# Performance work log

Measured on AMD Instinct MI355X. Metric: run time of the kernel, lower is better.

The kernel has to match this reference:

```python
import jax, jax.numpy as jnp
import numpy as np

V, CTX, D, L, H = 50257, 2048, 768, 12, 12
HD = D // H
EPS = 1e-5


def _ln(x, w, b):
    mu = jnp.mean(x, axis=-1, keepdims=True)
    var = jnp.mean(jnp.square(x - mu), axis=-1, keepdims=True)
    return (x - mu) * jax.lax.rsqrt(var + EPS) * w + b


def setup_inputs() -> dict:
    key = jax.random.key(0)
    ks = jax.random.split(key, 8)
    s = 0.02  # init std, matches _init_weights
    return {
        "idx": jax.random.randint(ks[0], (2, 2048), 0, V),
        "wte": jax.random.normal(ks[1], (V, D), jnp.float32) * s,
        "wpe": jax.random.normal(ks[2], (CTX, D), jnp.float32) * s,
        "ln1_w": jnp.ones((L, D), jnp.float32),
        "ln1_b": jnp.zeros((L, D), jnp.float32),
        "qkv_w": jax.random.normal(ks[3], (L, 3 * D, D), jnp.float32) * s,
        "out_w": jax.random.normal(ks[4], (L, D, D), jnp.float32) * s,
        "ln2_w": jnp.ones((L, D), jnp.float32),
        "ln2_b": jnp.zeros((L, D), jnp.float32),
        "fc1_w": jax.random.normal(ks[5], (L, 4 * D, D), jnp.float32) * s,
        "fc2_w": jax.random.normal(ks[6], (L, D, 4 * D), jnp.float32) * s,
        "lnf_w": jnp.ones((D,), jnp.float32),
        "lnf_b": jnp.zeros((D,), jnp.float32),
    }


def reference(idx, wte, wpe, ln1_w, ln1_b, qkv_w, out_w, ln2_w, ln2_b,
              fc1_w, fc2_w, lnf_w, lnf_b):
    B, S = idx.shape
    x = wte[idx] + wpe[:S][None]  # [B,S,D]
    causal = jnp.tril(jnp.ones((S, S), bool))  # [S,S]
    scale = 1.0 / np.sqrt(HD)

    def block(x, p):
        l1w, l1b, qkvw, ow, l2w, l2b, f1w, f2w = p
        h = _ln(x, l1w, l1b)
        qkv = h @ qkvw.T  # [B,S,3D]
        q, k, v = jnp.split(qkv, 3, axis=-1)
        q = q.reshape(B, S, H, HD)
        k = k.reshape(B, S, H, HD)
        v = v.reshape(B, S, H, HD)
        scores = jnp.einsum("bqhd,bkhd->bhqk", q, k) * scale
        scores = jnp.where(causal, scores, -jnp.inf)
        attn = jax.nn.softmax(scores, axis=-1)
        ctx = jnp.einsum("bhqk,bkhd->bqhd", attn, v).reshape(B, S, D)
        x = x + ctx @ ow.T
        h2 = _ln(x, l2w, l2b)
        mlp = jax.nn.gelu(h2 @ f1w.T, approximate=False) @ f2w.T
        return x + mlp, None

    x, _ = jax.lax.scan(block, x, (ln1_w, ln1_b, qkv_w, out_w, ln2_w, ln2_b, fc1_w, fc2_w))
    x = _ln(x, lnf_w, lnf_b)
    logits = x @ wte.T  # tied lm_head
    return logits
```

## Files before the change

kernel.cpp:

```cpp
#include <hip/hip_runtime.h>
#include <hip/hip_bf16.h>
#include <math.h>

typedef __attribute__((ext_vector_type(4))) float f32x4;
typedef __attribute__((ext_vector_type(8))) short bf16x8;
typedef __attribute__((ext_vector_type(4))) float float4v;
typedef unsigned short u16;
typedef unsigned int u32;

#define DIM 768
#define SEQ 2048
#define NTOK 4096
#define NH 12
#define NL 12
#define VOCAB 50257

__device__ __forceinline__ u16 f2bf(float f) {
  union { float f; u32 u; } c; c.f = f;
  u32 u = c.u;
  u32 r = u + 0x7fffu + ((u >> 16) & 1u);
  return (u16)(r >> 16);
}

__device__ __forceinline__ float fexp2(float x) {
#if __has_builtin(__builtin_amdgcn_exp2f)
  return __builtin_amdgcn_exp2f(x);
#else
  return exp2f(x);
#endif
}

__device__ __forceinline__ f32x4 mfma_bf16(bf16x8 a, bf16x8 b, f32x4 c) {
  return __builtin_amdgcn_mfma_f32_16x16x32_bf16(a, b, c, 0, 0, 0);
}

__device__ __forceinline__ void gload_lds16(const u16* g, u16* l) {
  __builtin_amdgcn_global_load_lds((const __attribute__((address_space(1))) u32*)g,
                                   (__attribute__((address_space(3))) u32*)l, 16, 0, 0);
}

__global__ void embed_k(const int* __restrict__ idx, const float* __restrict__ wte,
                        const float* __restrict__ wpe, float* __restrict__ x) {
  int t = blockIdx.x * 256 + threadIdx.x;
  int n = t / 192, c = t % 192;
  int tok = idx[n];
  float4v a = ((const float4v*)wte)[(size_t)tok * 192 + c];
  float4v p = ((const float4v*)wpe)[(size_t)(n & (SEQ - 1)) * 192 + c];
  ((float4v*)x)[t] = a + p;
}

__global__ __launch_bounds__(256) void ln_k(const float* __restrict__ x,
                                            const float* __restrict__ w,
                                            const float* __restrict__ b,
                                            u16* __restrict__ out) {
  int lane = threadIdx.x & 63;
  int row = blockIdx.x * 4 + (threadIdx.x >> 6);
  const float4v* xr = (const float4v*)(x + (size_t)row * DIM);
  float4v v[3];
#pragma unroll
  for (int i = 0; i < 3; ++i) v[i] = xr[i * 64 + lane];
  float s = 0.f;
#pragma unroll
  for (int i = 0; i < 3; ++i)
#pragma unroll
    for (int j = 0; j < 4; ++j) s += v[i][j];
#pragma unroll
  for (int o = 1; o < 64; o <<= 1) s += __shfl_xor(s, o);
  float mu = s * (1.f / 768.f);
  float vs = 0.f;
#pragma unroll
  for (int i = 0; i < 3; ++i)
#pragma unroll
    for (int j = 0; j < 4; ++j) { float d = v[i][j] - mu; vs += d * d; }
#pragma unroll
  for (int o = 1; o < 64; o <<= 1) vs += __shfl_xor(vs, o);
  float rs = rsqrtf(vs * (1.f / 768.f) + 1e-5f);
  u16* orow = out + (size_t)row * DIM;
#pragma unroll
  for (int i = 0; i < 3; ++i) {
    float4v wv = ((const float4v*)w)[i * 64 + lane];
    float4v bv = ((const float4v*)b)[i * 64 + lane];
    float y0 = (v[i][0] - mu) * rs * wv[0] + bv[0];
    float y1 = (v[i][1] - mu) * rs * wv[1] + bv[1];
    float y2 = (v[i][2] - mu) * rs * wv[2] + bv[2];
    float y3 = (v[i][3] - mu) * rs * wv[3] + bv[3];
    uint2 pk;
    pk.x = (u32)f2bf(y0) | ((u32)f2bf(y1) << 16);
    pk.y = (u32)f2bf(y2) | ((u32)f2bf(y3) << 16);
    ((uint2*)orow)[i * 64 + lane] = pk;
  }
}

__global__ void cvt_k(const float* __restrict__ src, u16* __restrict__ dst, int n4) {
  int stride = gridDim.x * blockDim.x;
  for (int i = blockIdx.x * blockDim.x + threadIdx.x; i < n4; i += stride) {
    float4v v = ((const float4v*)src)[i];
    uint2 pk;
    pk.x = (u32)f2bf(v[0]) | ((u32)f2bf(v[1]) << 16);
    pk.y = (u32)f2bf(v[2]) | ((u32)f2bf(v[3]) << 16);
    ((uint2*)dst)[i] = pk;
  }
}

template <int EPI>
__global__ __launch_bounds__(256) void gemm_bt(const u16* __restrict__ A,
                                               const u16* __restrict__ W, int Mdim,
                                               int Kdim, u16* __restrict__ outb,
                                               float* __restrict__ resid) {
  __shared__ u16 lA[128 * 64];
  __shared__ u16 lW[128 * 64];
  const int m0 = blockIdx.y * 128;
  const int n0 = blockIdx.x * 128;
  const int tid = threadIdx.x;
  const int lane = tid & 63, wv = tid >> 6;
  const int wr = wv >> 1, wc = wv & 1;
  const int lr = lane & 15, hi = lane >> 4;

  f32x4 acc[4][4];
#pragma unroll
  for (int i = 0; i < 4; ++i)
#pragma unroll
    for (int j = 0; j < 4; ++j) acc[i][j] = (f32x4){0.f, 0.f, 0.f, 0.f};

  const int s_row = tid >> 3;
  const int s_col = (tid & 7) * 8;
  int wrow[4];
#pragma unroll
  for (int it = 0; it < 4; ++it) {
    int r = m0 + s_row + it * 32;
    wrow[it] = (r < Mdim) ? r : (Mdim - 1);
  }

  for (int k0 = 0; k0 < Kdim; k0 += 64) {
    __syncthreads();
#pragma unroll
    for (int it = 0; it < 4; ++it) {
      gload_lds16(A + (size_t)(n0 + s_row + it * 32) * Kdim + k0 + s_col,
                  &lA[(s_row + it * 32) * 64 + s_col]);
      gload_lds16(W + (size_t)wrow[it] * Kdim + k0 + s_col,
                  &lW[(s_row + it * 32) * 64 + s_col]);
    }
    __syncthreads();
#pragma unroll
    for (int kk = 0; kk < 2; ++kk) {
      bf16x8 af[4], wf[4];
#pragma unroll
      for (int i = 0; i < 4; ++i)
        af[i] = *(const bf16x8*)(&lA[(wr * 64 + i * 16 + lr) * 64 + kk * 32 + hi * 8]);
#pragma unroll
      for (int j = 0; j < 4; ++j)
        wf[j] = *(const bf16x8*)(&lW[(wc * 64 + j * 16 + lr) * 64 + kk * 32 + hi * 8]);
#pragma unroll
      for (int i = 0; i < 4; ++i)
#pragma unroll
        for (int j = 0; j < 4; ++j) acc[i][j] = mfma_bf16(af[i], wf[j], acc[i][j]);
    }
  }

#pragma unroll
  for (int i = 0; i < 4; ++i) {
#pragma unroll
    for (int j = 0; j < 4; ++j) {
      int nb = n0 + wr * 64 + i * 16 + hi * 4;
      int m = m0 + wc * 64 + j * 16 + lr;
#pragma unroll
      for (int r = 0; r < 4; ++r) {
        float val = acc[i][j][r];
        size_t o = (size_t)(nb + r) * Mdim + m;
        if (EPI == 0) {
          if (m < Mdim) outb[o] = f2bf(val);
        } else if (EPI == 1) {
          float g = 0.5f * val * (1.f + erff(val * 0.70710678118f));
          outb[o] = f2bf(g);
        } else if (EPI == 2) {
          resid[o] += val;
        } else {
          if (m < Mdim) resid[o] = val;
        }
      }
    }
  }
}

__global__ __launch_bounds__(256) void vtrans_k(const u16* __restrict__ qkv,
                                                u16* __restrict__ vT) {
  __shared__ u16 t[64][65];
  int bh = blockIdx.y;
  int b = bh / NH, h = bh % NH;
  int s0 = blockIdx.x * 64;
  int tid = threadIdx.x;
  int col = tid & 63, row0 = tid >> 6;
#pragma unroll
  for (int it = 0; it < 16; ++it) {
    int srow = row0 + it * 4;
    t[srow][col] = qkv[(size_t)(b * SEQ + s0 + srow) * 2304 + 1536 + h * 64 + col];
  }
  __syncthreads();
#pragma unroll
  for (int it = 0; it < 16; ++it) {
    int drow = row0 + it * 4;
    vT[((size_t)bh * 64 + drow) * SEQ + s0 + col] = t[col][drow];
  }
}

__global__ __launch_bounds__(512) void flash_k(const u16* __restrict__ qkv,
                                               const u16* __restrict__ vT,
                                               u16* __restrict__ ctx) {
  const int tid = threadIdx.x;
  const int lane = tid & 63, wq = tid >> 6;
  const int lr = lane & 15, hi = lane >> 4;
  const int pi = blockIdx.x;
  const int bh = blockIdx.y;
  const int b = bh / NH, h = bh % NH;
  const size_t rowb = (size_t)b * SEQ;
  const float SCL = 0.125f * 1.44269504f;

  __shared__ u16 lK[64 * 80];
  __shared__ u16 lV[64 * 80];
  __shared__ u16 Pb[8][16 * 40];
  u16* P = Pb[wq];

  const int s_row = tid >> 3;
  const int s_col = (tid & 7) * 8;
  const u16* kSrc = qkv + rowb * 2304 + 768 + h * 64;
  const u16* vSrc = vT + ((size_t)bh * 64 + s_row) * SEQ;

#pragma unroll
  for (int pass = 0; pass < 2; ++pass) {
    const int qb = (pass == 0 ? (15 - pi) : pi) * 128;
    const int qa = qb + wq * 16;

    const u16* Qp = qkv + (rowb + qa + lr) * 2304 + h * 64 + hi * 8;
    bf16x8 qf0 = *(const bf16x8*)(Qp);
    bf16x8 qf1 = *(const bf16x8*)(Qp + 32);

    f32x4 o[4];
    float mreg[4], lreg[4];
#pragma unroll
    for (int ct = 0; ct < 4; ++ct) o[ct] = (f32x4){0.f, 0.f, 0.f, 0.f};
#pragma unroll
    for (int r = 0; r < 4; ++r) { mreg[r] = -1e30f; lreg[r] = 0.f; }

    const int kTop = qb + 127;
    bf16x8 kreg = *(const bf16x8*)(kSrc + (size_t)s_row * 2304 + s_col);
    bf16x8 vreg = *(const bf16x8*)(vSrc + s_col);

    for (int k0 = 0; k0 <= kTop; k0 += 64) {
      __syncthreads();
      *(bf16x8*)(&lK[s_row * 80 + s_col]) = kreg;
      *(bf16x8*)(&lV[s_row * 80 + s_col]) = vreg;
      __syncthreads();
      if (k0 + 64 <= kTop) {
        kreg = *(const bf16x8*)(kSrc + (size_t)(k0 + 64 + s_row) * 2304 + s_col);
        vreg = *(const bf16x8*)(vSrc + k0 + 64 + s_col);
      }
      if (k0 <= qa + 15) {
#pragma unroll
        for (int ks = 0; ks < 2; ++ks) {
          const int kg = k0 + ks * 32;
          f32x4 s0 = (f32x4){0.f, 0.f, 0.f, 0.f}, s1 = (f32x4){0.f, 0.f, 0.f, 0.f};
          {
            bf16x8 ka = *(const bf16x8*)(&lK[(ks * 32 + lr) * 80 + hi * 8]);
            bf16x8 kc = *(const bf16x8*)(&lK[(ks * 32 + lr) * 80 + hi * 8 + 32]);
            s0 = mfma_bf16(qf0, ka, s0);
            s0 = mfma_bf16(qf1, kc, s0);
            bf16x8 kd = *(const bf16x8*)(&lK[(ks * 32 + 16 + lr) * 80 + hi * 8]);
            bf16x8 ke = *(const bf16x8*)(&lK[(ks * 32 + 16 + lr) * 80 + hi * 8 + 32]);
            s1 = mfma_bf16(qf0, kd, s1);
            s1 = mfma_bf16(qf1, ke, s1);
          }
          float cor[4];
#pragma unroll
          for (int r = 0; r < 4; ++r) {
            int qrow = qa + hi * 4 + r;
            float v0 = s0[r] * SCL;
            if (kg + lr > qrow) v0 = -1e30f;
            float v1 = s1[r] * SCL;
            if (kg + 16 + lr > qrow) v1 = -1e30f;
            s0[r] = v0; s1[r] = v1;
            float m = fmaxf(v0, v1);
            m = fmaxf(m, __shfl_xor(m, 1));
            m = fmaxf(m, __shfl_xor(m, 2));
            m = fmaxf(m, __shfl_xor(m, 4));
            m = fmaxf(m, __shfl_xor(m, 8));
            float mnew = fmaxf(mreg[r], m);
            cor[r] = fexp2(mreg[r] - mnew);
            mreg[r] = mnew;
          }
#pragma unroll
          for (int r = 0; r < 4; ++r) {
            float p0 = fexp2(s0[r] - mreg[r]);
            float p1 = fexp2(s1[r] - mreg[r]);
            lreg[r] = lreg[r] * cor[r] + p0 + p1;
            P[(hi * 4 + r) * 40 + lr] = f2bf(p0);
            P[(hi * 4 + r) * 40 + 16 + lr] = f2bf(p1);
#pragma unroll
            for (int ct = 0; ct < 4; ++ct) o[ct][r] *= cor[r];
          }
          bf16x8 pa = *(const bf16x8*)(&P[lr * 40 + hi * 8]);
#pragma unroll
          for (int ct = 0; ct < 4; ++ct) {
            bf16x8 vf = *(const bf16x8*)(&lV[(ct * 16 + lr) * 80 + ks * 32 + hi * 8]);
            o[ct] = mfma_bf16(pa, vf, o[ct]);
          }
        }
      }
    }

    float lfin[4];
#pragma unroll
    for (int r = 0; r < 4; ++r) {
      float l = lreg[r];
      l += __shfl_xor(l, 1);
      l += __shfl_xor(l, 2);
      l += __shfl_xor(l, 4);
      l += __shfl_xor(l, 8);
      lfin[r] = 1.f / l;
    }
#pragma unroll
    for (int ct = 0; ct < 4; ++ct)
#pragma unroll
      for (int r = 0; r < 4; ++r) {
        float ov = o[ct][r] * lfin[r];
        size_t n = rowb + qa + hi * 4 + r;
        ctx[n * DIM + h * 64 + ct * 16 + lr] = f2bf(ov);
      }
  }
}

extern "C" void kernel_launch(void* const* d_in, const int* in_sizes, int n_in,
                              void* d_out, int out_size, void* d_ws, size_t ws_size,
                              hipStream_t stream) {
  (void)in_sizes; (void)n_in; (void)out_size; (void)ws_size;
  const int* idx = (const int*)d_in[0];
  const float* wte = (const float*)d_in[1];
  const float* wpe = (const float*)d_in[2];
  const float* ln1w = (const float*)d_in[3];
  const float* ln1b = (const float*)d_in[4];
  const float* qkvw = (const float*)d_in[5];
  const float* outw = (const float*)d_in[6];
  const float* ln2w = (const float*)d_in[7];
  const float* ln2b = (const float*)d_in[8];
  const float* fc1w = (const float*)d_in[9];
  const float* fc2w = (const float*)d_in[10];
  const float* lnfw = (const float*)d_in[11];
  const float* lnfb = (const float*)d_in[12];
  float* out = (float*)d_out;

  char* ws = (char*)d_ws;
  size_t off = 0;
  auto carve = [&](size_t bytes) {
    char* p = ws + off;
    off += (bytes + 255) & ~(size_t)255;
    return p;
  };
  u16* hb = (u16*)carve((size_t)NTOK * DIM * 2);
  u16* wteb = (u16*)carve((size_t)VOCAB * DIM * 2);

  char* os = (char*)d_out;
  size_t ooff = 0;
  auto ocarve = [&](size_t bytes) {
    char* p = os + ooff;
    ooff += (bytes + 255) & ~(size_t)255;
    return p;
  };
  float* xb = (float*)ocarve((size_t)NTOK * DIM * 4);
  u16* qkvb = (u16*)ocarve((size_t)NTOK * 3 * DIM * 2);
  u16* ctxb = (u16*)ocarve((size_t)NTOK * DIM * 2);
  u16* mhb = (u16*)ocarve((size_t)NTOK * 4 * DIM * 2);
  u16* vTb = (u16*)ocarve((size_t)2 * NH * 64 * SEQ * 2);
  u16* qkvwb = (u16*)ocarve((size_t)NL * 1769472 * 2);
  u16* outwb = (u16*)ocarve((size_t)NL * 589824 * 2);
  u16* fc1wb = (u16*)ocarve((size_t)NL * 2359296 * 2);
  u16* fc2wb = (u16*)ocarve((size_t)NL * 2359296 * 2);

  cvt_k<<<2048, 256, 0, stream>>>(qkvw, qkvwb, NL * 442368);
  cvt_k<<<2048, 256, 0, stream>>>(outw, outwb, NL * 147456);
  cvt_k<<<2048, 256, 0, stream>>>(fc1w, fc1wb, NL * 589824);
  cvt_k<<<2048, 256, 0, stream>>>(fc2w, fc2wb, NL * 589824);
  cvt_k<<<2048, 256, 0, stream>>>(wte, wteb, 9649344);

  embed_k<<<3072, 256, 0, stream>>>(idx, wte, wpe, xb);

  for (int l = 0; l < NL; ++l) {
    ln_k<<<1024, 256, 0, stream>>>(xb, ln1w + l * DIM, ln1b + l * DIM, hb);
    gemm_bt<0><<<dim3(32, 18), 256, 0, stream>>>(hb, qkvwb + (size_t)l * 1769472,
                                                 2304, 768, qkvb, nullptr);
    vtrans_k<<<dim3(32, 24), 256, 0, stream>>>(qkvb, vTb);
    flash_k<<<dim3(8, 24), 512, 0, stream>>>(qkvb, vTb, ctxb);
    gemm_bt<2><<<dim3(32, 6), 256, 0, stream>>>(ctxb, outwb + (size_t)l * 589824,
                                                768, 768, nullptr, xb);
    ln_k<<<1024, 256, 0, stream>>>(xb, ln2w + l * DIM, ln2b + l * DIM, hb);
    gemm_bt<1><<<dim3(32, 24), 256, 0, stream>>>(hb, fc1wb + (size_t)l * 2359296,
                                                 3072, 768, mhb, nullptr);
    gemm_bt<2><<<dim3(32, 6), 256, 0, stream>>>(mhb, fc2wb + (size_t)l * 2359296,
                                                768, 3072, nullptr, xb);
  }

  ln_k<<<1024, 256, 0, stream>>>(xb, lnfw, lnfb, hb);
  gemm_bt<3><<<dim3(32, 393), 256, 0, stream>>>(hb, wteb, VOCAB, 768, nullptr, out);
}
```

Baseline: 4.414 ms.

## Add 256x256-tile double-buffered GEMM for QKV, FC1 and LM-head

Introduces a new 512-thread GEMM kernel with 256x256 output tiles, double-buffered LDS staging through direct global-to-LDS loads, and MFMA priority hints. It replaces the 128x128 gemm_bt for the QKV, FC1 and tied LM-head projections. The larger tiles raise arithmetic intensity and cut redundant global loads. In exchange the grids are smaller (144, 192 and 3152 blocks), which may underfill the GPU's compute units for the per-layer GEMMs. LDS use is high (128 KB per block), limiting occupancy to one block per CU.

```diff
diff --git a/kernel.cpp b/kernel.cpp
--- a/kernel.cpp
+++ b/kernel.cpp
@@ -174,6 +174,107 @@
           outb[o] = f2bf(g);
         } else if (EPI == 2) {
           resid[o] += val;
+        } else {
+          if (m < Mdim) resid[o] = val;
+        }
+      }
+    }
+  }
+}
+
+template <int EPI>
+__global__ __launch_bounds__(512) void gemm256(const u16* __restrict__ A,
+                                               const u16* __restrict__ W, int Mdim,
+                                               int Kdim, u16* __restrict__ outb,
+                                               float* __restrict__ resid) {
+  __shared__ u16 lA[2][256 * 64];
+  __shared__ u16 lB[2][256 * 64];
+  const int n0 = blockIdx.x * 256;
+  const int m0 = blockIdx.y * 256;
+  const int tid = threadIdx.x;
+  const int lane = tid & 63, wid = tid >> 6;
+  const int wr = wid >> 2, wc = wid & 3;
+  const int lr = lane & 15, hi = lane >> 4;
+
+  const int s_row = tid >> 3;
+  const int s_col = (tid & 7) * 8;
+  int wrow[4];
+#pragma unroll
+  for (int it = 0; it < 4; ++it) {
+    int r = m0 + s_row + it * 64;
+    wrow[it] = (r < Mdim) ? r : (Mdim - 1);
+  }
+
+  f32x4 acc[8][4];
+#pragma unroll
+  for (int i = 0; i < 8; ++i)
+#pragma unroll
+    for (int j = 0; j < 4; ++j) acc[i][j] = (f32x4){0.f, 0.f, 0.f, 0.f};
+
+  const int nt = Kdim >> 6;
+
+  auto stage = [&](int kt, int buf) {
+    const int k0 = kt * 64;
+#pragma unroll
+    for (int it = 0; it < 4; ++it)
+      gload_lds16(A + (size_t)(n0 + s_row + it * 64) * Kdim + k0 + s_col,
+                  &lA[buf][(s_row + it * 64) * 64 + s_col]);
+#pragma unroll
+    for (int it = 0; it < 4; ++it)
+      gload_lds16(W + (size_t)wrow[it] * Kdim + k0 + s_col,
+                  &lB[buf][(s_row + it * 64) * 64 + s_col]);
+  };
+
+  stage(0, 0);
+  stage(1, 1);
+  asm volatile("s_waitcnt vmcnt(8)" ::: "memory");
+  __builtin_amdgcn_s_barrier();
+
+  for (int t = 0; t < nt; ++t) {
+    const int cur = t & 1;
+    const u16* la = lA[cur];
+    const u16* lb = lB[cur];
+#pragma unroll
+    for (int kk = 0; kk < 2; ++kk) {
+      bf16x8 af[8], wf[4];
+#pragma unroll
+      for (int i = 0; i < 8; ++i)
+        af[i] = *(const bf16x8*)(&la[(wr * 128 + i * 16 + lr) * 64 + kk * 32 + hi * 8]);
+#pragma unroll
+      for (int j = 0; j < 4; ++j)
+        wf[j] = *(const bf16x8*)(&lb[(wc * 64 + j * 16 + lr) * 64 + kk * 32 + hi * 8]);
+      __builtin_amdgcn_s_setprio(1);
+#pragma unroll
+      for (int i = 0; i < 8; ++i)
+#pragma unroll
+        for (int j = 0; j < 4; ++j) acc[i][j] = mfma_bf16(af[i], wf[j], acc[i][j]);
+      __builtin_amdgcn_s_setprio(0);
+    }
+    __builtin_amdgcn_s_barrier();
+    if (t + 2 < nt) {
+      stage(t + 2, cur);
+      asm volatile("s_waitcnt vmcnt(8)" ::: "memory");
+    } else if (t + 1 < nt) {
+      asm volatile("s_waitcnt vmcnt(0)" ::: "memory");
+    }
+    __builtin_amdgcn_s_barrier();
+  }
+
+#pragma unroll
+  for (int i = 0; i < 8; ++i) {
+#pragma unroll
+    for (int j = 0; j < 4; ++j) {
+      int nb = n0 + wr * 128 + i * 16 + hi * 4;
+      int m = m0 + wc * 64 + j * 16 + lr;
+#pragma unroll
+      for (int r = 0; r < 4; ++r) {
+        float val = acc[i][j][r];
+        size_t o = (size_t)(nb + r) * Mdim + m;
+        if (EPI == 0) {
+          if (m < Mdim) outb[o] = f2bf(val);
+        } else if (EPI == 1) {
+          float g = 0.5f * val * (1.f + erff(val * 0.70710678118f));
+          outb[o] = f2bf(g);
         } else {
           if (m < Mdim) resid[o] = val;
         }
@@ -384,19 +485,19 @@
 
   for (int l = 0; l < NL; ++l) {
     ln_k<<<1024, 256, 0, stream>>>(xb, ln1w + l * DIM, ln1b + l * DIM, hb);
-    gemm_bt<0><<<dim3(32, 18), 256, 0, stream>>>(hb, qkvwb + (size_t)l * 1769472,
-                                                 2304, 768, qkvb, nullptr);
+    gemm256<0><<<dim3(16, 9), 512, 0, stream>>>(hb, qkvwb + (size_t)l * 1769472,
+                                                2304, 768, qkvb, nullptr);
     vtrans_k<<<dim3(32, 24), 256, 0, stream>>>(qkvb, vTb);
     flash_k<<<dim3(8, 24), 512, 0, stream>>>(qkvb, vTb, ctxb);
     gemm_bt<2><<<dim3(32, 6), 256, 0, stream>>>(ctxb, outwb + (size_t)l * 589824,
                                                 768, 768, nullptr, xb);
     ln_k<<<1024, 256, 0, stream>>>(xb, ln2w + l * DIM, ln2b + l * DIM, hb);
-    gemm_bt<1><<<dim3(32, 24), 256, 0, stream>>>(hb, fc1wb + (size_t)l * 2359296,
+    gemm256<1><<<dim3(16, 12), 512, 0, stream>>>(hb, fc1wb + (size_t)l * 2359296,
                                                  3072, 768, mhb, nullptr);
     gemm_bt<2><<<dim3(32, 6), 256, 0, stream>>>(mhb, fc2wb + (size_t)l * 2359296,
                                                 768, 3072, nullptr, xb);
   }
 
   ln_k<<<1024, 256, 0, stream>>>(xb, lnfw, lnfb, hb);
-  gemm_bt<3><<<dim3(32, 393), 256, 0, stream>>>(hb, wteb, VOCAB, 768, nullptr, out);
-}
+  gemm256<3><<<dim3(16, 197), 512, 0, stream>>>(hb, wteb, VOCAB, 768, nullptr, out);
+}
```

After: 4.277 ms. -3.1%, faster.
